# Optimization experiments

Hardware: AMD Instinct MI355X
Metric: run time of the kernel (lower is better)

The kernel has to match this reference:

```python
import jax, jax.numpy as jnp
import numpy as np

EPS_BN = 1e-5
EPS_NORM = 1e-12


def setup_inputs() -> dict:
    dim, mid, k = 128, 32, 3
    b, h, w = 8, 128, 128
    key = jax.random.key(0)
    ks = jax.random.split(key, 16)
    s = 0.05
    return {
        "x": jax.random.normal(ks[0], (b, dim, h, w), jnp.float32),
        "w_spatial_in": jax.random.normal(ks[1], (dim, dim), jnp.float32) * s,
        "w_dw_spatial": jax.random.normal(ks[2], (dim, 1, k), jnp.float32) * s,
        "w_spatial_out": jax.random.normal(ks[3], (dim, dim), jnp.float32) * s,
        "w_ch_in": jax.random.normal(ks[4], (dim, dim), jnp.float32) * s,
        "w_ch_dw": jax.random.normal(ks[5], (dim, 1, k), jnp.float32) * s,
        "w_ch_out": jax.random.normal(ks[6], (dim, dim), jnp.float32) * s,
        "w_mlp1": jax.random.normal(ks[7], (mid, dim), jnp.float32) * s,
        "b_mlp1": jax.random.normal(ks[8], (mid,), jnp.float32) * s,
        "w_mlp2": jax.random.normal(ks[9], (dim, mid), jnp.float32) * s,
        "b_mlp2": jax.random.normal(ks[10], (dim,), jnp.float32) * s,
        "diff_weight": jnp.float32(1.0),
        "bn_gamma": jnp.ones((dim,), jnp.float32),
        "bn_beta": jnp.zeros((dim,), jnp.float32),
        "w_out_proj": jax.random.normal(ks[11], (dim, dim), jnp.float32) * s,
    }


def _dwconv1d(seq, wk):
    # seq: [b, c, L], wk: [c, 1, k] depthwise, 'same' padding
    c = seq.shape[1]
    k = wk.shape[-1]
    return jax.lax.conv_general_dilated(
        seq, wk, window_strides=(1,), padding=[(k // 2, k // 2)],
        dimension_numbers=("NCH", "OIH", "NCH"), feature_group_count=c)


def _ocs_forward(x, w_spatial_in, w_dw_spatial, w_spatial_out,
                 w_ch_in, w_ch_dw, w_ch_out,
                 w_mlp1, b_mlp1, w_mlp2, b_mlp2,
                 diff_weight, bn_gamma, bn_beta, w_out_proj):
    b, c, h, w = x.shape
    L = h * w
    alpha = beta = eta = 1.0

    # ---- scan indices (4 orders) ----
    idx_row = jnp.arange(L)
    gy, gx = jnp.meshgrid(jnp.arange(h), jnp.arange(w), indexing="ij")
    idx_col = (gx * h + gy).reshape(-1)
    orders = [idx_row, idx_row[::-1], idx_col, idx_col[::-1]]

    x_seq0 = x.reshape(b, c, L).transpose(0, 2, 1)  # [b, L, c]

    def scan(idx):
        s = x_seq0[:, idx]                                   # gather   [b,L,c]
        s = jnp.einsum("blc,oc->blo", s, w_spatial_in)       # linear
        s = _dwconv1d(s.transpose(0, 2, 1), w_dw_spatial)    # dw conv  [b,c,L]
        s = jnp.einsum("bcl,oc->blo", s, w_spatial_out)      # linear   [b,L,c]
        s = s.at[:, idx].set(s[:, jnp.arange(L)]) if False else s[:, jnp.argsort(idx)]  # scatter back (inverse perm)
        return s.transpose(0, 2, 1).reshape(b, c, h, w)

    y_sp = (scan(orders[0]) + scan(orders[1]) + scan(orders[2]) + scan(orders[3])) * 0.25

    # ---- channel branch ----
    seq = x.reshape(b, c, L)
    seq = jnp.einsum("oc,bcl->bol", w_ch_in, seq)
    seq = _dwconv1d(seq, w_ch_dw)
    seq = jnp.einsum("oc,bcl->bol", w_ch_out, seq)
    gap = x.mean((2, 3))                                     # [b,c]
    gap = gap / jnp.maximum(jnp.linalg.norm(gap, axis=1, keepdims=True), EPS_NORM)
    m = jnp.einsum("bi,bj->bij", gap, gap)                   # [b,c,c]
    seq_agg = jnp.einsum("bij,bjl->bil", m, seq)             # [b,c,L]
    h1 = jax.nn.silu(jnp.einsum("mc,bcl->bml", w_mlp1, seq_agg) + b_mlp1[None, :, None])
    y_ch = (jnp.einsum("cm,bml->bcl", w_mlp2, h1) + b_mlp2[None, :, None]).reshape(b, c, h, w)

    # ---- difference branch (reflect-pad 4-neighbor abs diff) ----
    p = jnp.pad(x, ((0, 0), (0, 0), (1, 1), (1, 1)), mode="reflect")
    cx = p[:, :, 1:-1, 1:-1]
    diff = (jnp.abs(cx - p[:, :, 1:-1, :-2]) + jnp.abs(cx - p[:, :, 1:-1, 2:])
            + jnp.abs(cx - p[:, :, :-2, 1:-1]) + jnp.abs(cx - p[:, :, 2:, 1:-1])) * 0.25
    y_diff = x + diff_weight * diff

    # ---- combine, 1x1 proj, batchnorm (training-mode batch stats) ----
    y = alpha * y_sp + beta * y_ch + eta * y_diff
    y = jnp.einsum("oc,bchw->bohw", w_out_proj, y)
    mu = y.mean((0, 2, 3))
    var = y.var((0, 2, 3))
    y = (y - mu[None, :, None, None]) * jax.lax.rsqrt(var + EPS_BN)[None, :, None, None]
    y = y * bn_gamma[None, :, None, None] + bn_beta[None, :, None, None]
    return y


def reference(x, w_spatial_in, w_dw_spatial, w_spatial_out, w_ch_in, w_ch_dw,
              w_ch_out, w_mlp1, b_mlp1, w_mlp2, b_mlp2, diff_weight,
              bn_gamma, bn_beta, w_out_proj):
    return _ocs_forward(x, w_spatial_in, w_dw_spatial, w_spatial_out,
                        w_ch_in, w_ch_dw, w_ch_out, w_mlp1, b_mlp1,
                        w_mlp2, b_mlp2, diff_weight, bn_gamma, bn_beta,
                        w_out_proj)
```

## Files before the change

kernel.cpp:

```cpp
#include <hip/hip_runtime.h>
#include <hip/hip_bf16.h>

#define C 128
#define L 16384
#define B 8
#define MID 32
#define NBL (B * L)

typedef unsigned short ushort_t;
typedef __attribute__((ext_vector_type(8))) short s8v;
typedef __attribute__((ext_vector_type(4))) float f4v;

__device__ __forceinline__ unsigned short f2bf(float f) {
    union { float f; unsigned int u; } a; a.f = f;
    unsigned int u = a.u;
    return (unsigned short)((u + 0x7fffu + ((u >> 16) & 1u)) >> 16);
}

__device__ __forceinline__ void load8(const ushort_t* p, float* f) {
    uint4 u = *(const uint4*)p;
    f[0] = __uint_as_float(u.x << 16); f[1] = __uint_as_float(u.x & 0xffff0000u);
    f[2] = __uint_as_float(u.y << 16); f[3] = __uint_as_float(u.y & 0xffff0000u);
    f[4] = __uint_as_float(u.z << 16); f[5] = __uint_as_float(u.z & 0xffff0000u);
    f[6] = __uint_as_float(u.w << 16); f[7] = __uint_as_float(u.w & 0xffff0000u);
}

__device__ __forceinline__ void zero8(float* f) {
#pragma unroll
    for (int j = 0; j < 8; j++) f[j] = 0.f;
}

__device__ __forceinline__ void store8(ushort_t* p, const float* f) {
    union { ushort_t h[8]; uint4 q; } u;
#pragma unroll
    for (int j = 0; j < 8; j++) u.h[j] = f2bf(f[j]);
    *(uint4*)p = u.q;
}

__device__ __forceinline__ void ld8f(const float* p, float* f) {
    float4 a = *(const float4*)p;
    float4 b = *(const float4*)(p + 4);
    f[0] = a.x; f[1] = a.y; f[2] = a.z; f[3] = a.w;
    f[4] = b.x; f[5] = b.y; f[6] = b.z; f[7] = b.w;
}

__global__ __launch_bounds__(256) void k_cvt(const float* __restrict__ x,
                                             ushort_t* __restrict__ xb,
                                             float* __restrict__ gap) {
    __shared__ float xs[64][129];
    const int bid = blockIdx.x;
    const int b = bid >> 8;
    const int l0 = (bid & 255) * 64;
    const int tid = threadIdx.x;
    const int c = tid >> 1, h = tid & 1;
    const float* src = x + ((size_t)(b * C + c)) * L + l0 + h * 32;
    float s = 0.f;
#pragma unroll
    for (int j = 0; j < 8; j++) {
        float4 v = *(const float4*)(src + j * 4);
        s += (v.x + v.y) + (v.z + v.w);
        int lb = h * 32 + j * 4;
        xs[lb + 0][c] = v.x; xs[lb + 1][c] = v.y;
        xs[lb + 2][c] = v.z; xs[lb + 3][c] = v.w;
    }
    s += __shfl_xor(s, 1);
    if (h == 0) atomicAdd(&gap[b * C + c], s);
    __syncthreads();
    const int l = tid & 63, quarter = tid >> 6, cb = quarter * 32;
    union { ushort_t hh[32]; uint4 q[4]; } u;
#pragma unroll
    for (int k = 0; k < 32; k++) u.hh[k] = f2bf(xs[l][cb + k]);
    uint4* dst = (uint4*)(xb + ((size_t)(b * L + l0 + l)) * C + cb);
#pragma unroll
    for (int k = 0; k < 4; k++) dst[k] = u.q[k];
}

__global__ __launch_bounds__(128) void k_prep_b(const float* __restrict__ gap,
                                                const float* __restrict__ w1,
                                                const float* __restrict__ Wco,
                                                float* __restrict__ a,
                                                float* __restrict__ gw) {
    int b = blockIdx.x, c = threadIdx.x;
    __shared__ float gl[C];
    __shared__ float red[C];
    float v = gap[b * C + c] * (1.f / (float)L);
    red[c] = v * v;
    __syncthreads();
    for (int w = 64; w > 0; w >>= 1) {
        if (c < w) red[c] += red[c + w];
        __syncthreads();
    }
    float nrm = fmaxf(sqrtf(red[0]), 1e-12f);
    float gc = v / nrm;
    gl[c] = gc;
    __syncthreads();
    if (c < MID) {
        float s = 0.f;
        for (int k = 0; k < C; k++) s = fmaf(w1[c * C + k], gl[k], s);
        a[b * MID + c] = s;
    }
    {
        float s = 0.f;
        for (int k = 0; k < C; k++) s = fmaf(gl[k], Wco[k * C + c], s);
        gw[b * C + c] = s;
    }
}

__global__ __launch_bounds__(128) void k_prep_w(const float* __restrict__ Win,
                                                const float* __restrict__ Wci,
                                                const float* __restrict__ Wproj,
                                                const float* __restrict__ Wout,
                                                const float* __restrict__ w2,
                                                const float* __restrict__ b2,
                                                const float* __restrict__ wds,
                                                const float* __restrict__ wcd,
                                                ushort_t* __restrict__ Wio,
                                                ushort_t* __restrict__ Wcat,
                                                float* __restrict__ bp,
                                                float* __restrict__ kwS,
                                                float* __restrict__ kw1,
                                                float* __restrict__ kd0,
                                                float* __restrict__ kd1,
                                                float* __restrict__ kd2) {
    int o = blockIdx.x, c = threadIdx.x;
    __shared__ float pr[C];
    pr[c] = Wproj[o * C + c];
    __syncthreads();
    Wio[o * C + c] = f2bf(Win[o * C + c]);
    Wio[(C + o) * C + c] = f2bf(Wci[o * C + c]);
    float s = 0.f;
    for (int k = 0; k < C; k++) s = fmaf(pr[k], Wout[k * C + c], s);
    Wcat[o * 288 + c] = f2bf(s);
    Wcat[o * 288 + 128 + c] = f2bf(pr[c]);
    if (c < MID) {
        float s2 = 0.f;
        for (int k = 0; k < C; k++) s2 = fmaf(pr[k], w2[k * MID + c], s2);
        Wcat[o * 288 + 256 + c] = f2bf(s2);
    }
    if (c == 0) {
        float s3 = 0.f;
        for (int k = 0; k < C; k++) s3 = fmaf(pr[k], b2[k], s3);
        bp[o] = s3;
    }
    if (o == 0) {
        kwS[c] = 0.25f * (wds[3 * c] + wds[3 * c + 2]);
        kw1[c] = wds[3 * c + 1];
        kd0[c] = wcd[3 * c];
        kd1[c] = wcd[3 * c + 1];
        kd2[c] = wcd[3 * c + 2];
    }
}

__global__ __launch_bounds__(512, 1) void k_gemm1(const ushort_t* __restrict__ xb,
                                                  const ushort_t* __restrict__ Wio,
                                                  ushort_t* __restrict__ tu) {
    __shared__ ushort_t wl[128 * 136];
    const int tid = threadIdx.x;
    const int bid = blockIdx.x;
    const int b = bid >> 8;
    const int ms = (bid >> 7) & 1;
    const int lt = bid & 127;
    {
        int row = tid >> 2, qq = tid & 3;
        const uint4* s4 = (const uint4*)(Wio + (ms * C + row) * C + qq * 32);
        uint4* d4 = (uint4*)(wl + row * 136 + qq * 32);
        d4[0] = s4[0]; d4[1] = s4[1]; d4[2] = s4[2]; d4[3] = s4[3];
    }
    __syncthreads();
    const int wave = tid >> 6, lane = tid & 63;
    const int l0 = lt * 128 + wave * 16;
    const int n = lane & 15, q = lane >> 4;
    const ushort_t* brow = xb + ((size_t)(b * L + l0 + n)) * C + q * 8;
    s8v bfrag[4];
#pragma unroll
    for (int ks = 0; ks < 4; ks++) bfrag[ks] = *(const s8v*)(brow + ks * 32);
    f4v acc[8];
#pragma unroll
    for (int i = 0; i < 8; i++) acc[i] = (f4v){0.f, 0.f, 0.f, 0.f};
#pragma unroll
    for (int ks = 0; ks < 4; ks++) {
#pragma unroll
        for (int mt = 0; mt < 8; mt++) {
            s8v af = *(const s8v*)(wl + (mt * 16 + n) * 136 + ks * 32 + q * 8);
            acc[mt] = __builtin_amdgcn_mfma_f32_16x16x32_bf16(af, bfrag[ks], acc[mt], 0, 0, 0);
        }
    }
    ushort_t* orow = tu + ((size_t)(b * L + l0 + n)) * 256 + ms * C + q * 4;
#pragma unroll
    for (int mt = 0; mt < 8; mt++) {
        union { ushort_t h[4]; uint2 q2; } u;
#pragma unroll
        for (int i = 0; i < 4; i++) u.h[i] = f2bf(acc[mt][i]);
        *(uint2*)(orow + mt * 16) = u.q2;
    }
}

__global__ __launch_bounds__(256) void k_mid(const ushort_t* __restrict__ tu,
                                             const ushort_t* __restrict__ xb,
                                             const float* __restrict__ kwS,
                                             const float* __restrict__ kw1,
                                             const float* __restrict__ kd0,
                                             const float* __restrict__ kd1,
                                             const float* __restrict__ kd2,
                                             const float* __restrict__ gw,
                                             const float* __restrict__ a,
                                             const float* __restrict__ b1,
                                             const float* __restrict__ pdw,
                                             ushort_t* __restrict__ Kb) {
    const int tid = threadIdx.x;
    const int cc = tid & 15, p = tid >> 4;
    const int bid = blockIdx.x;
    const int b = bid >> 10;
    const int l = (bid & 1023) * 16 + p;
    const int y = l >> 7, xg = l & 127;
    const int c0 = cc * 8;
    const size_t rb = (size_t)b * L;

    const int rL = (l > 0) ? (l - 1) : -1;
    const int rR = (l < L - 1) ? (l + 1) : -1;
    const int rU = (y > 0) ? (l - 128) : ((xg > 0) ? (16256 + xg - 1) : -1);
    const int rD = (y < 127) ? (l + 128) : ((xg < 127) ? (xg + 1) : -1);
    const int sL = (xg > 0) ? (l - 1) : (l + 1);
    const int sR = (xg < 127) ? (l + 1) : (l - 1);
    const int sU = (y > 0) ? (l - 128) : (l + 128);
    const int sD = (y < 127) ? (l + 128) : (l - 128);

    float tC[8], tLe[8], tRi[8], tUp[8], tDo[8];
    load8(tu + (rb + l) * 256 + c0, tC);
    if (rL >= 0) load8(tu + (rb + rL) * 256 + c0, tLe); else zero8(tLe);
    if (rR >= 0) load8(tu + (rb + rR) * 256 + c0, tRi); else zero8(tRi);
    if (rU >= 0) load8(tu + (rb + rU) * 256 + c0, tUp); else zero8(tUp);
    if (rD >= 0) load8(tu + (rb + rD) * 256 + c0, tDo); else zero8(tDo);

    float uC[8], uL8[8], uR8[8];
    load8(tu + (rb + l) * 256 + 128 + c0, uC);
    if (rL >= 0) load8(tu + (rb + rL) * 256 + 128 + c0, uL8); else zero8(uL8);
    if (rR >= 0) load8(tu + (rb + rR) * 256 + 128 + c0, uR8); else zero8(uR8);

    float xC[8], xL8[8], xR8[8], xU8[8], xD8[8];
    load8(xb + (rb + l) * C + c0, xC);
    load8(xb + (rb + sL) * C + c0, xL8);
    load8(xb + (rb + sR) * C + c0, xR8);
    load8(xb + (rb + sU) * C + c0, xU8);
    load8(xb + (rb + sD) * C + c0, xD8);

    float kS[8], k1[8], d0[8], d1[8], d2[8], gv[8];
    ld8f(kwS + c0, kS); ld8f(kw1 + c0, k1);
    ld8f(kd0 + c0, d0); ld8f(kd1 + c0, d1); ld8f(kd2 + c0, d2);
    ld8f(gw + b * C + c0, gv);
    const float dwt = pdw[0] * 0.25f;

    float ct[8], yd[8];
    float s1 = 0.f;
#pragma unroll
    for (int j = 0; j < 8; j++) {
        ct[j] = kS[j] * ((tLe[j] + tRi[j]) + (tUp[j] + tDo[j])) + k1[j] * tC[j];
        float vv = d0[j] * uL8[j] + d1[j] * uC[j] + d2[j] * uR8[j];
        s1 = fmaf(gv[j], vv, s1);
        float cen = xC[j];
        float d = fabsf(cen - xL8[j]) + fabsf(cen - xR8[j]) +
                  fabsf(cen - xU8[j]) + fabsf(cen - xD8[j]);
        yd[j] = fmaf(dwt, d, cen);
    }
    s1 += __shfl_xor(s1, 1);
    s1 += __shfl_xor(s1, 2);
    s1 += __shfl_xor(s1, 4);
    s1 += __shfl_xor(s1, 8);

    ushort_t* kr = Kb + (rb + l) * 288;
    store8(kr + c0, ct);
    store8(kr + 128 + c0, yd);
    if (cc < 4) {
        float av[8], bv[8], sv[8];
        ld8f(a + b * MID + cc * 8, av);
        ld8f(b1 + cc * 8, bv);
#pragma unroll
        for (int j = 0; j < 8; j++) {
            float pre = fmaf(av[j], s1, bv[j]);
            sv[j] = pre / (1.f + __expf(-pre));
        }
        store8(kr + 256 + cc * 8, sv);
    }
}

__global__ __launch_bounds__(512, 1) void k_gemm2(const ushort_t* __restrict__ Kb,
                                                  const ushort_t* __restrict__ Wcat,
                                                  const float* __restrict__ bp,
                                                  float* __restrict__ outp) {
    __shared__ ushort_t wl[64 * 296];
    const int tid = threadIdx.x;
    const int bid = blockIdx.x;
    const int b = bid >> 8;
    const int ms = (bid >> 7) & 1;
    const int lt = bid & 127;
    for (int i = 0; i < 5; i++) {
        int idx = tid + i * 512;
        if (idx < 2304) {
            int row = idx / 36, col = idx - row * 36;
            *(uint4*)(wl + row * 296 + col * 8) =
                *(const uint4*)(Wcat + (ms * 64 + row) * 288 + col * 8);
        }
    }
    __syncthreads();
    const int wave = tid >> 6, lane = tid & 63;
    const int l0 = lt * 128 + wave * 16;
    const int n = lane & 15, q = lane >> 4;
    const ushort_t* brow = Kb + ((size_t)(b * L + l0 + n)) * 288 + q * 8;
    f4v acc[4];
#pragma unroll
    for (int i = 0; i < 4; i++) acc[i] = (f4v){0.f, 0.f, 0.f, 0.f};
#pragma unroll
    for (int ks = 0; ks < 9; ks++) {
        s8v bf_ = *(const s8v*)(brow + ks * 32);
#pragma unroll
        for (int mt = 0; mt < 4; mt++) {
            s8v af = *(const s8v*)(wl + (mt * 16 + n) * 296 + ks * 32 + q * 8);
            acc[mt] = __builtin_amdgcn_mfma_f32_16x16x32_bf16(af, bf_, acc[mt], 0, 0, 0);
        }
    }
#pragma unroll
    for (int mt = 0; mt < 4; mt++) {
        int o0 = ms * 64 + mt * 16 + q * 4;
        float4 bv = *(const float4*)(bp + o0);
        float ba[4] = {bv.x, bv.y, bv.z, bv.w};
#pragma unroll
        for (int i = 0; i < 4; i++) {
            outp[((size_t)(b * C + o0 + i)) * L + l0 + n] = acc[mt][i] + ba[i];
        }
    }
}

__global__ __launch_bounds__(256) void k_bnstats2(const float* __restrict__ outp,
                                                  float* __restrict__ stats) {
    const int bo = blockIdx.x;
    const int o = bo & (C - 1);
    const float4* p = (const float4*)(outp + (size_t)bo * L);
    float s = 0.f, sq = 0.f;
    for (int i = threadIdx.x; i < L / 4; i += 256) {
        float4 v = p[i];
        s += (v.x + v.y) + (v.z + v.w);
        sq += v.x * v.x + v.y * v.y + v.z * v.z + v.w * v.w;
    }
    __shared__ float rs[256], rq[256];
    rs[threadIdx.x] = s; rq[threadIdx.x] = sq;
    __syncthreads();
    for (int w = 128; w > 0; w >>= 1) {
        if (threadIdx.x < w) {
            rs[threadIdx.x] += rs[threadIdx.x + w];
            rq[threadIdx.x] += rq[threadIdx.x + w];
        }
        __syncthreads();
    }
    if (threadIdx.x == 0) {
        atomicAdd(&stats[o], rs[0]);
        atomicAdd(&stats[C + o], rq[0]);
    }
}

__global__ void k_bnfin(const float* __restrict__ stats, const float* __restrict__ gamma,
                        const float* __restrict__ beta, float* __restrict__ scsh) {
    int o = threadIdx.x;
    float n = (float)NBL;
    float mu = stats[o] / n;
    float var = stats[C + o] / n - mu * mu;
    float sc = gamma[o] * rsqrtf(var + 1e-5f);
    scsh[o] = sc;
    scsh[C + o] = fmaf(-mu, sc, beta[o]);
}

__global__ __launch_bounds__(256) void k_bnapply(float* __restrict__ outp,
                                                 const float* __restrict__ scsh) {
    int bo = blockIdx.x;
    int o = bo & (C - 1);
    float sc = scsh[o], sh = scsh[C + o];
    float4* p = (float4*)(outp + (size_t)bo * L);
    for (int i = threadIdx.x; i < L / 4; i += 256) {
        float4 v = p[i];
        v.x = fmaf(v.x, sc, sh);
        v.y = fmaf(v.y, sc, sh);
        v.z = fmaf(v.z, sc, sh);
        v.w = fmaf(v.w, sc, sh);
        p[i] = v;
    }
}

extern "C" void kernel_launch(void* const* d_in, const int* in_sizes, int n_in,
                              void* d_out, int out_size, void* d_ws, size_t ws_size,
                              hipStream_t stream) {
    const float* x = (const float*)d_in[0];
    const float* Win = (const float*)d_in[1];
    const float* wds = (const float*)d_in[2];
    const float* Wout = (const float*)d_in[3];
    const float* Wci = (const float*)d_in[4];
    const float* wcd = (const float*)d_in[5];
    const float* Wco = (const float*)d_in[6];
    const float* w1 = (const float*)d_in[7];
    const float* b1 = (const float*)d_in[8];
    const float* w2 = (const float*)d_in[9];
    const float* b2 = (const float*)d_in[10];
    const float* pdw = (const float*)d_in[11];
    const float* gamma = (const float*)d_in[12];
    const float* beta = (const float*)d_in[13];
    const float* Wproj = (const float*)d_in[14];

    char* wsb = (char*)d_ws;
    ushort_t* xb = (ushort_t*)wsb;
    ushort_t* tu = (ushort_t*)(wsb + 33554432);
    ushort_t* Kb = (ushort_t*)(wsb + 100663296);
    char* S = wsb + 176160768;
    float* gap  = (float*)(S + 0);
    float* stats= (float*)(S + 4096);
    float* scsh = (float*)(S + 5120);
    float* a    = (float*)(S + 6144);
    float* gw   = (float*)(S + 7168);
    float* bp   = (float*)(S + 11264);
    float* kwS  = (float*)(S + 11776);
    float* kw1  = (float*)(S + 12288);
    float* kd0  = (float*)(S + 12800);
    float* kd1  = (float*)(S + 13312);
    float* kd2  = (float*)(S + 13824);
    ushort_t* Wio  = (ushort_t*)(S + 14336);
    ushort_t* Wcat = (ushort_t*)(S + 79872);
    float* outp = (float*)d_out;

    hipMemsetAsync(S, 0, 5120, stream);
    k_cvt<<<2048, 256, 0, stream>>>(x, xb, gap);
    k_prep_b<<<8, 128, 0, stream>>>(gap, w1, Wco, a, gw);
    k_prep_w<<<128, 128, 0, stream>>>(Win, Wci, Wproj, Wout, w2, b2, wds, wcd,
                                      Wio, Wcat, bp, kwS, kw1, kd0, kd1, kd2);
    k_gemm1<<<2048, 512, 0, stream>>>(xb, Wio, tu);
    k_mid<<<8192, 256, 0, stream>>>(tu, xb, kwS, kw1, kd0, kd1, kd2, gw, a, b1, pdw, Kb);
    k_gemm2<<<2048, 512, 0, stream>>>(Kb, Wcat, bp, outp);
    k_bnstats2<<<1024, 256, 0, stream>>>(outp, stats);
    k_bnfin<<<1, 128, 0, stream>>>(stats, gamma, beta, scsh);
    k_bnapply<<<1024, 256, 0, stream>>>(outp, scsh);
}
```

Measured before the change: 313.0 us.

## Fuse stencil mid-stage into output GEMM and fold BN stats into epilogue

The separate stencil/elementwise kernel that wrote an intermediate bf16 K buffer is merged into the second GEMM. The GEMM now builds its B-operand fragments on the fly from tu and xb neighbors, with each block handling one image row and all 128 output channels. The BN statistics pass is folded into the GEMM epilogue by re-reading the just-written row and doing atomic accumulation, and the channel depthwise weights are pre-multiplied into gd0..gd2. This removes the K buffer's write and read traffic plus a full re-read of the output, in exchange for redundant neighbor loads inside the GEMM, a larger LDS weight tile and more register pressure.

```diff
diff --git a/kernel.cpp b/kernel.cpp
--- a/kernel.cpp
+++ b/kernel.cpp
@@ -28,13 +28,6 @@
 __device__ __forceinline__ void zero8(float* f) {
 #pragma unroll
     for (int j = 0; j < 8; j++) f[j] = 0.f;
-}
-
-__device__ __forceinline__ void store8(ushort_t* p, const float* f) {
-    union { ushort_t h[8]; uint4 q; } u;
-#pragma unroll
-    for (int j = 0; j < 8; j++) u.h[j] = f2bf(f[j]);
-    *(uint4*)p = u.q;
 }
 
 __device__ __forceinline__ void ld8f(const float* p, float* f) {
@@ -78,8 +71,11 @@
 __global__ __launch_bounds__(128) void k_prep_b(const float* __restrict__ gap,
                                                 const float* __restrict__ w1,
                                                 const float* __restrict__ Wco,
+                                                const float* __restrict__ wcd,
                                                 float* __restrict__ a,
-                                                float* __restrict__ gw) {
+                                                float* __restrict__ gd0,
+                                                float* __restrict__ gd1,
+                                                float* __restrict__ gd2) {
     int b = blockIdx.x, c = threadIdx.x;
     __shared__ float gl[C];
     __shared__ float red[C];
@@ -102,7 +98,9 @@
     {
         float s = 0.f;
         for (int k = 0; k < C; k++) s = fmaf(gl[k], Wco[k * C + c], s);
-        gw[b * C + c] = s;
+        gd0[b * C + c] = s * wcd[3 * c];
+        gd1[b * C + c] = s * wcd[3 * c + 1];
+        gd2[b * C + c] = s * wcd[3 * c + 2];
     }
 }
 
@@ -113,15 +111,11 @@
                                                 const float* __restrict__ w2,
                                                 const float* __restrict__ b2,
                                                 const float* __restrict__ wds,
-                                                const float* __restrict__ wcd,
                                                 ushort_t* __restrict__ Wio,
                                                 ushort_t* __restrict__ Wcat,
                                                 float* __restrict__ bp,
                                                 float* __restrict__ kwS,
-                                                float* __restrict__ kw1,
-                                                float* __restrict__ kd0,
-                                                float* __restrict__ kd1,
-                                                float* __restrict__ kd2) {
+                                                float* __restrict__ kw1) {
     int o = blockIdx.x, c = threadIdx.x;
     __shared__ float pr[C];
     pr[c] = Wproj[o * C + c];
@@ -145,9 +139,6 @@
     if (o == 0) {
         kwS[c] = 0.25f * (wds[3 * c] + wds[3 * c + 2]);
         kw1[c] = wds[3 * c + 1];
-        kd0[c] = wcd[3 * c];
-        kd1[c] = wcd[3 * c + 1];
-        kd2[c] = wcd[3 * c + 2];
     }
 }
 
@@ -195,25 +186,37 @@
     }
 }
 
-__global__ __launch_bounds__(256) void k_mid(const ushort_t* __restrict__ tu,
-                                             const ushort_t* __restrict__ xb,
-                                             const float* __restrict__ kwS,
-                                             const float* __restrict__ kw1,
-                                             const float* __restrict__ kd0,
-                                             const float* __restrict__ kd1,
-                                             const float* __restrict__ kd2,
-                                             const float* __restrict__ gw,
-                                             const float* __restrict__ a,
-                                             const float* __restrict__ b1,
-                                             const float* __restrict__ pdw,
-                                             ushort_t* __restrict__ Kb) {
+__global__ __launch_bounds__(512, 4) void k_gemm2f(const ushort_t* __restrict__ tu,
+                                                   const ushort_t* __restrict__ xb,
+                                                   const ushort_t* __restrict__ Wcat,
+                                                   const float* __restrict__ kwS,
+                                                   const float* __restrict__ kw1,
+                                                   const float* __restrict__ gd0,
+                                                   const float* __restrict__ gd1,
+                                                   const float* __restrict__ gd2,
+                                                   const float* __restrict__ a,
+                                                   const float* __restrict__ b1,
+                                                   const float* __restrict__ pdw,
+                                                   const float* __restrict__ bp,
+                                                   float* __restrict__ outp,
+                                                   float* __restrict__ stats) {
+    __shared__ ushort_t wl[128 * 296];
     const int tid = threadIdx.x;
-    const int cc = tid & 15, p = tid >> 4;
     const int bid = blockIdx.x;
-    const int b = bid >> 10;
-    const int l = (bid & 1023) * 16 + p;
-    const int y = l >> 7, xg = l & 127;
-    const int c0 = cc * 8;
+    const int b = bid >> 7;
+    const int y = bid & 127;
+
+#pragma unroll
+    for (int i = 0; i < 9; i++) {
+        int idx = tid + i * 512;
+        int row = idx / 36, col = idx - row * 36;
+        *(uint4*)(wl + row * 296 + col * 8) = *(const uint4*)(Wcat + row * 288 + col * 8);
+    }
+
+    const int wave = tid >> 6, lane = tid & 63;
+    const int n = lane & 15, q = lane >> 4;
+    const int xg = wave * 16 + n;
+    const int l = y * 128 + xg;
     const size_t rb = (size_t)b * L;
 
     const int rL = (l > 0) ? (l - 1) : -1;
@@ -225,135 +228,144 @@
     const int sU = (y > 0) ? (l - 128) : (l + 128);
     const int sD = (y < 127) ? (l + 128) : (l - 128);
 
-    float tC[8], tLe[8], tRi[8], tUp[8], tDo[8];
-    load8(tu + (rb + l) * 256 + c0, tC);
-    if (rL >= 0) load8(tu + (rb + rL) * 256 + c0, tLe); else zero8(tLe);
-    if (rR >= 0) load8(tu + (rb + rR) * 256 + c0, tRi); else zero8(tRi);
-    if (rU >= 0) load8(tu + (rb + rU) * 256 + c0, tUp); else zero8(tUp);
-    if (rD >= 0) load8(tu + (rb + rD) * 256 + c0, tDo); else zero8(tDo);
-
-    float uC[8], uL8[8], uR8[8];
-    load8(tu + (rb + l) * 256 + 128 + c0, uC);
-    if (rL >= 0) load8(tu + (rb + rL) * 256 + 128 + c0, uL8); else zero8(uL8);
-    if (rR >= 0) load8(tu + (rb + rR) * 256 + 128 + c0, uR8); else zero8(uR8);
-
-    float xC[8], xL8[8], xR8[8], xU8[8], xD8[8];
-    load8(xb + (rb + l) * C + c0, xC);
-    load8(xb + (rb + sL) * C + c0, xL8);
-    load8(xb + (rb + sR) * C + c0, xR8);
-    load8(xb + (rb + sU) * C + c0, xU8);
-    load8(xb + (rb + sD) * C + c0, xD8);
-
-    float kS[8], k1[8], d0[8], d1[8], d2[8], gv[8];
-    ld8f(kwS + c0, kS); ld8f(kw1 + c0, k1);
-    ld8f(kd0 + c0, d0); ld8f(kd1 + c0, d1); ld8f(kd2 + c0, d2);
-    ld8f(gw + b * C + c0, gv);
+    float s1 = 0.f;
+    {
+        const ushort_t* pC = tu + (rb + l) * 256 + 128 + q * 32;
+        const ushort_t* pL = (rL >= 0) ? (tu + (rb + rL) * 256 + 128 + q * 32) : (const ushort_t*)0;
+        const ushort_t* pR = (rR >= 0) ? (tu + (rb + rR) * 256 + 128 + q * 32) : (const ushort_t*)0;
+#pragma unroll
+        for (int j = 0; j < 4; j++) {
+            float uC[8], uL8[8], uR8[8], g0[8], g1[8], g2[8];
+            load8(pC + j * 8, uC);
+            if (pL) load8(pL + j * 8, uL8); else zero8(uL8);
+            if (pR) load8(pR + j * 8, uR8); else zero8(uR8);
+            const int cb2 = b * C + q * 32 + j * 8;
+            ld8f(gd0 + cb2, g0); ld8f(gd1 + cb2, g1); ld8f(gd2 + cb2, g2);
+#pragma unroll
+            for (int j2 = 0; j2 < 8; j2++) {
+                s1 = fmaf(g0[j2], uL8[j2], s1);
+                s1 = fmaf(g1[j2], uC[j2], s1);
+                s1 = fmaf(g2[j2], uR8[j2], s1);
+            }
+        }
+    }
+    s1 += __shfl_xor(s1, 16);
+    s1 += __shfl_xor(s1, 32);
+
     const float dwt = pdw[0] * 0.25f;
 
-    float ct[8], yd[8];
-    float s1 = 0.f;
-#pragma unroll
-    for (int j = 0; j < 8; j++) {
-        ct[j] = kS[j] * ((tLe[j] + tRi[j]) + (tUp[j] + tDo[j])) + k1[j] * tC[j];
-        float vv = d0[j] * uL8[j] + d1[j] * uC[j] + d2[j] * uR8[j];
-        s1 = fmaf(gv[j], vv, s1);
-        float cen = xC[j];
-        float d = fabsf(cen - xL8[j]) + fabsf(cen - xR8[j]) +
-                  fabsf(cen - xU8[j]) + fabsf(cen - xD8[j]);
-        yd[j] = fmaf(dwt, d, cen);
-    }
-    s1 += __shfl_xor(s1, 1);
-    s1 += __shfl_xor(s1, 2);
-    s1 += __shfl_xor(s1, 4);
-    s1 += __shfl_xor(s1, 8);
-
-    ushort_t* kr = Kb + (rb + l) * 288;
-    store8(kr + c0, ct);
-    store8(kr + 128 + c0, yd);
-    if (cc < 4) {
-        float av[8], bv[8], sv[8];
-        ld8f(a + b * MID + cc * 8, av);
-        ld8f(b1 + cc * 8, bv);
+    f4v acc[8];
+#pragma unroll
+    for (int i = 0; i < 8; i++) acc[i] = (f4v){0.f, 0.f, 0.f, 0.f};
+
+    __syncthreads();
+
+    {
+        const ushort_t* ptC = tu + (rb + l) * 256;
+        const ushort_t* ptL = (rL >= 0) ? (tu + (rb + rL) * 256) : (const ushort_t*)0;
+        const ushort_t* ptR = (rR >= 0) ? (tu + (rb + rR) * 256) : (const ushort_t*)0;
+        const ushort_t* ptU = (rU >= 0) ? (tu + (rb + rU) * 256) : (const ushort_t*)0;
+        const ushort_t* ptD = (rD >= 0) ? (tu + (rb + rD) * 256) : (const ushort_t*)0;
+#pragma unroll
+        for (int ks = 0; ks < 4; ks++) {
+            const int c0 = ks * 32 + q * 8;
+            float tC[8], tLe[8], tRi[8], tUp[8], tDo[8], kS[8], k1[8];
+            load8(ptC + c0, tC);
+            if (ptL) load8(ptL + c0, tLe); else zero8(tLe);
+            if (ptR) load8(ptR + c0, tRi); else zero8(tRi);
+            if (ptU) load8(ptU + c0, tUp); else zero8(tUp);
+            if (ptD) load8(ptD + c0, tDo); else zero8(tDo);
+            ld8f(kwS + c0, kS); ld8f(kw1 + c0, k1);
+            union { ushort_t h[8]; s8v v; } bf;
+#pragma unroll
+            for (int j = 0; j < 8; j++) {
+                float ct = kS[j] * ((tLe[j] + tRi[j]) + (tUp[j] + tDo[j])) + k1[j] * tC[j];
+                bf.h[j] = f2bf(ct);
+            }
+#pragma unroll
+            for (int mt = 0; mt < 8; mt++) {
+                s8v af = *(const s8v*)(wl + (mt * 16 + n) * 296 + ks * 32 + q * 8);
+                acc[mt] = __builtin_amdgcn_mfma_f32_16x16x32_bf16(af, bf.v, acc[mt], 0, 0, 0);
+            }
+        }
+    }
+
+    {
+        const ushort_t* pxC = xb + (rb + l) * C;
+        const ushort_t* pxL = xb + (rb + sL) * C;
+        const ushort_t* pxR = xb + (rb + sR) * C;
+        const ushort_t* pxU = xb + (rb + sU) * C;
+        const ushort_t* pxD = xb + (rb + sD) * C;
+#pragma unroll
+        for (int ks = 0; ks < 4; ks++) {
+            const int c0 = ks * 32 + q * 8;
+            float xC[8], xL8[8], xR8[8], xU8[8], xD8[8];
+            load8(pxC + c0, xC);
+            load8(pxL + c0, xL8);
+            load8(pxR + c0, xR8);
+            load8(pxU + c0, xU8);
+            load8(pxD + c0, xD8);
+            union { ushort_t h[8]; s8v v; } bf;
+#pragma unroll
+            for (int j = 0; j < 8; j++) {
+                float cen = xC[j];
+                float d = fabsf(cen - xL8[j]) + fabsf(cen - xR8[j]) +
+                          fabsf(cen - xU8[j]) + fabsf(cen - xD8[j]);
+                bf.h[j] = f2bf(fmaf(dwt, d, cen));
+            }
+#pragma unroll
+            for (int mt = 0; mt < 8; mt++) {
+                s8v af = *(const s8v*)(wl + (mt * 16 + n) * 296 + (4 + ks) * 32 + q * 8);
+                acc[mt] = __builtin_amdgcn_mfma_f32_16x16x32_bf16(af, bf.v, acc[mt], 0, 0, 0);
+            }
+        }
+    }
+
+    {
+        float av[8], bv[8];
+        ld8f(a + b * MID + q * 8, av);
+        ld8f(b1 + q * 8, bv);
+        union { ushort_t h[8]; s8v v; } bf;
 #pragma unroll
         for (int j = 0; j < 8; j++) {
             float pre = fmaf(av[j], s1, bv[j]);
-            sv[j] = pre / (1.f + __expf(-pre));
-        }
-        store8(kr + 256 + cc * 8, sv);
-    }
-}
-
-__global__ __launch_bounds__(512, 1) void k_gemm2(const ushort_t* __restrict__ Kb,
-                                                  const ushort_t* __restrict__ Wcat,
-                                                  const float* __restrict__ bp,
-                                                  float* __restrict__ outp) {
-    __shared__ ushort_t wl[64 * 296];
-    const int tid = threadIdx.x;
-    const int bid = blockIdx.x;
-    const int b = bid >> 8;
-    const int ms = (bid >> 7) & 1;
-    const int lt = bid & 127;
-    for (int i = 0; i < 5; i++) {
-        int idx = tid + i * 512;
-        if (idx < 2304) {
-            int row = idx / 36, col = idx - row * 36;
-            *(uint4*)(wl + row * 296 + col * 8) =
-                *(const uint4*)(Wcat + (ms * 64 + row) * 288 + col * 8);
-        }
-    }
-    __syncthreads();
-    const int wave = tid >> 6, lane = tid & 63;
-    const int l0 = lt * 128 + wave * 16;
-    const int n = lane & 15, q = lane >> 4;
-    const ushort_t* brow = Kb + ((size_t)(b * L + l0 + n)) * 288 + q * 8;
-    f4v acc[4];
-#pragma unroll
-    for (int i = 0; i < 4; i++) acc[i] = (f4v){0.f, 0.f, 0.f, 0.f};
-#pragma unroll
-    for (int ks = 0; ks < 9; ks++) {
-        s8v bf_ = *(const s8v*)(brow + ks * 32);
-#pragma unroll
-        for (int mt = 0; mt < 4; mt++) {
-            s8v af = *(const s8v*)(wl + (mt * 16 + n) * 296 + ks * 32 + q * 8);
-            acc[mt] = __builtin_amdgcn_mfma_f32_16x16x32_bf16(af, bf_, acc[mt], 0, 0, 0);
-        }
-    }
-#pragma unroll
-    for (int mt = 0; mt < 4; mt++) {
-        int o0 = ms * 64 + mt * 16 + q * 4;
-        float4 bv = *(const float4*)(bp + o0);
-        float ba[4] = {bv.x, bv.y, bv.z, bv.w};
+            bf.h[j] = f2bf(pre / (1.f + __expf(-pre)));
+        }
+#pragma unroll
+        for (int mt = 0; mt < 8; mt++) {
+            s8v af = *(const s8v*)(wl + (mt * 16 + n) * 296 + 256 + q * 8);
+            acc[mt] = __builtin_amdgcn_mfma_f32_16x16x32_bf16(af, bf.v, acc[mt], 0, 0, 0);
+        }
+    }
+
+#pragma unroll
+    for (int mt = 0; mt < 8; mt++) {
+        const int o0 = mt * 16 + q * 4;
+        float4 bv4 = *(const float4*)(bp + o0);
+        float ba[4] = {bv4.x, bv4.y, bv4.z, bv4.w};
 #pragma unroll
         for (int i = 0; i < 4; i++) {
-            outp[((size_t)(b * C + o0 + i)) * L + l0 + n] = acc[mt][i] + ba[i];
-        }
-    }
-}
-
-__global__ __launch_bounds__(256) void k_bnstats2(const float* __restrict__ outp,
-                                                  float* __restrict__ stats) {
-    const int bo = blockIdx.x;
-    const int o = bo & (C - 1);
-    const float4* p = (const float4*)(outp + (size_t)bo * L);
-    float s = 0.f, sq = 0.f;
-    for (int i = threadIdx.x; i < L / 4; i += 256) {
-        float4 v = p[i];
-        s += (v.x + v.y) + (v.z + v.w);
-        sq += v.x * v.x + v.y * v.y + v.z * v.z + v.w * v.w;
-    }
-    __shared__ float rs[256], rq[256];
-    rs[threadIdx.x] = s; rq[threadIdx.x] = sq;
-    __syncthreads();
-    for (int w = 128; w > 0; w >>= 1) {
-        if (threadIdx.x < w) {
-            rs[threadIdx.x] += rs[threadIdx.x + w];
-            rq[threadIdx.x] += rq[threadIdx.x + w];
-        }
-        __syncthreads();
-    }
-    if (threadIdx.x == 0) {
-        atomicAdd(&stats[o], rs[0]);
-        atomicAdd(&stats[C + o], rq[0]);
+            outp[((size_t)(b * C + o0 + i)) * L + l] = acc[mt][i] + ba[i];
+        }
+    }
+
+    __syncthreads();
+    {
+        const int o = tid >> 2, seg = tid & 3;
+        const float* pr = outp + ((size_t)(b * C + o)) * L + y * 128 + seg * 32;
+        float s = 0.f, sq = 0.f;
+#pragma unroll
+        for (int i = 0; i < 8; i++) {
+            float4 v = *(const float4*)(pr + i * 4);
+            s += (v.x + v.y) + (v.z + v.w);
+            sq += v.x * v.x + v.y * v.y + v.z * v.z + v.w * v.w;
+        }
+        s += __shfl_xor(s, 1); sq += __shfl_xor(sq, 1);
+        s += __shfl_xor(s, 2); sq += __shfl_xor(sq, 2);
+        if (seg == 0) {
+            atomicAdd(&stats[o], s);
+            atomicAdd(&stats[C + o], sq);
+        }
     }
 }
 
@@ -406,32 +418,29 @@
     char* wsb = (char*)d_ws;
     ushort_t* xb = (ushort_t*)wsb;
     ushort_t* tu = (ushort_t*)(wsb + 33554432);
-    ushort_t* Kb = (ushort_t*)(wsb + 100663296);
+    float* gd0 = (float*)(wsb + 100663296);
+    float* gd1 = (float*)(wsb + 100663296 + 4096);
+    float* gd2 = (float*)(wsb + 100663296 + 8192);
     char* S = wsb + 176160768;
     float* gap  = (float*)(S + 0);
     float* stats= (float*)(S + 4096);
     float* scsh = (float*)(S + 5120);
     float* a    = (float*)(S + 6144);
-    float* gw   = (float*)(S + 7168);
     float* bp   = (float*)(S + 11264);
     float* kwS  = (float*)(S + 11776);
     float* kw1  = (float*)(S + 12288);
-    float* kd0  = (float*)(S + 12800);
-    float* kd1  = (float*)(S + 13312);
-    float* kd2  = (float*)(S + 13824);
     ushort_t* Wio  = (ushort_t*)(S + 14336);
     ushort_t* Wcat = (ushort_t*)(S + 79872);
     float* outp = (float*)d_out;
 
     hipMemsetAsync(S, 0, 5120, stream);
     k_cvt<<<2048, 256, 0, stream>>>(x, xb, gap);
-    k_prep_b<<<8, 128, 0, stream>>>(gap, w1, Wco, a, gw);
-    k_prep_w<<<128, 128, 0, stream>>>(Win, Wci, Wproj, Wout, w2, b2, wds, wcd,
-                                      Wio, Wcat, bp, kwS, kw1, kd0, kd1, kd2);
+    k_prep_b<<<8, 128, 0, stream>>>(gap, w1, Wco, wcd, a, gd0, gd1, gd2);
+    k_prep_w<<<128, 128, 0, stream>>>(Win, Wci, Wproj, Wout, w2, b2, wds,
+                                      Wio, Wcat, bp, kwS, kw1);
     k_gemm1<<<2048, 512, 0, stream>>>(xb, Wio, tu);
-    k_mid<<<8192, 256, 0, stream>>>(tu, xb, kwS, kw1, kd0, kd1, kd2, gw, a, b1, pdw, Kb);
-    k_gemm2<<<2048, 512, 0, stream>>>(Kb, Wcat, bp, outp);
-    k_bnstats2<<<1024, 256, 0, stream>>>(outp, stats);
+    k_gemm2f<<<1024, 512, 0, stream>>>(tu, xb, Wcat, kwS, kw1, gd0, gd1, gd2,
+                                       a, b1, pdw, bp, outp, stats);
     k_bnfin<<<1, 128, 0, stream>>>(stats, gamma, beta, scsh);
     k_bnapply<<<1024, 256, 0, stream>>>(outp, scsh);
 }
```

Result: slower. 344.2 us (+10.0%).
